# Performance work log

Hardware: AMD Instinct MI355X
Metric: run time of the kernel (lower is better)

## Reference

```python
import jax, jax.numpy as jnp
import numpy as np

ALPHA = 0.1
STEPS = 4


def setup_inputs() -> dict:
    key = jax.random.key(0)
    x = jax.random.normal(key, (4, 8192, 1024), dtype=jnp.float32)
    return {"x": x}


def reference(x) -> jnp.ndarray:
    # CtaPostAttnMixer.forward, layout='bld', prefill, steps=4, alpha=0.1
    # Fixed-boundary 1D heat-diffusion stencil along the sequence dim.
    if x.shape[1] < 3:
        return x
    y = x.astype(jnp.float32)
    for _ in range(STEPS):
        # Laplacian on interior tokens: y[l+1] - 2 y[l] + y[l-1]
        lap = y[:, 2:, :] - 2.0 * y[:, 1:-1, :] + y[:, :-2, :]
        y = jnp.concatenate(
            [y[:, :1, :], y[:, 1:-1, :] + ALPHA * lap, y[:, -1:, :]], axis=1
        )
    return y.astype(x.dtype)
```

## Files before the change

### kernel.cpp

```cpp
#include <hip/hip_runtime.h>


namespace {

constexpr int Lr   = 8192;
constexpr int Dq   = 1024 / 4;
constexpr int Bn   = 4;
constexpr int R    = 32;
constexpr int WR   = R + 8;
constexpr int CW   = 32;
constexpr int RT   = Lr / R;
constexpr int CT   = Dq / CW;
constexpr int NXCD = 8;
constexpr int NWG  = RT * CT * Bn;

constexpr float WK0 = 0.4870f;
constexpr float WK1 = 0.2144f;
constexpr float WK2 = 0.0388f;
constexpr float WK3 = 0.0032f;
constexpr float WK4 = 0.0001f;

__device__ __forceinline__ float4 f4_add(float4 a, float4 b) {
    return make_float4(a.x + b.x, a.y + b.y, a.z + b.z, a.w + b.w);
}
__device__ __forceinline__ float4 f4_mul(float s, float4 a) {
    return make_float4(s * a.x, s * a.y, s * a.z, s * a.w);
}
__device__ __forceinline__ float4 f4_fma(float s, float4 a, float4 c) {
    return make_float4(fmaf(s, a.x, c.x), fmaf(s, a.y, c.y),
                       fmaf(s, a.z, c.z), fmaf(s, a.w, c.w));
}

__global__ __launch_bounds__(256, 7)
void mixer4_kernel(const float4* __restrict__ x, float4* __restrict__ y) {
    __shared__ float4 tile[WR][CW];

    const int lin = blockIdx.x;
    const int g   = (lin & (NXCD - 1)) * (NWG / NXCD) + (lin >> 3);
    const int rt  = g & (RT - 1);
    const int bc  = g >> 8;
    const int ct  = bc & (CT - 1);
    const int b   = bc >> 3;
    const int r0  = rt * R;

    const size_t origin = (size_t)b * Lr * Dq + (size_t)ct * CW;
    const float4* __restrict__ xt = x + origin;
    float4* __restrict__       yt = y + origin;

    const int lane = threadIdx.x & 63;
    const int wid  = threadIdx.x >> 6;

#pragma unroll
    for (int ii = 0; ii < 5; ++ii) {
        const int p = wid + ii * 4;
        int grow = r0 - 4 + 2 * p + (lane >> 5);
        grow = grow < 0 ? 0 : grow;
        grow = grow > Lr - 1 ? Lr - 1 : grow;
        const float4* src = xt + (size_t)grow * Dq + (lane & 31);
        __builtin_amdgcn_global_load_lds(
            (const __attribute__((address_space(1))) void*)src,
            (__attribute__((address_space(3))) void*)&tile[2 * p][0],
            16, 0, 0);
    }
    __syncthreads();

    const int c  = threadIdx.x & 31;
    const int gr = threadIdx.x >> 5;
    float4 win[12];
#pragma unroll
    for (int i = 0; i < 12; ++i) win[i] = tile[4 * gr + i][c];

    auto interior = [&](int j) {
        float4 acc = f4_mul(WK0, win[j + 4]);
        acc = f4_fma(WK1, f4_add(win[j + 3], win[j + 5]), acc);
        acc = f4_fma(WK2, f4_add(win[j + 2], win[j + 6]), acc);
        acc = f4_fma(WK3, f4_add(win[j + 1], win[j + 7]), acc);
        acc = f4_fma(WK4, f4_add(win[j + 0], win[j + 8]), acc);
        yt[(size_t)(r0 + 4 * gr + j) * Dq + c] = acc;
    };

    const bool low  = (rt == 0)      && (gr == 0);
    const bool high = (rt == RT - 1) && (gr == 7);

    if (low) {
        yt[0 * (size_t)Dq + c] = win[4];
        {
            float4 o = f4_mul(0.2986f, win[4]);
            o = f4_fma(0.4482f, win[5], o);
            o = f4_fma(0.2112f, win[6], o);
            o = f4_fma(0.0387f, win[7], o);
            o = f4_fma(0.0032f, win[8], o);
            o = f4_fma(0.0001f, win[9], o);
            yt[1 * (size_t)Dq + c] = o;
        }
        {
            float4 o = f4_mul(0.0454f, win[4]);
            o = f4_fma(0.2112f, win[5], o);
            o = f4_fma(0.4869f, win[6], o);
            o = f4_fma(0.2144f, win[7], o);
            o = f4_fma(0.0388f, win[8], o);
            o = f4_fma(0.0032f, win[9], o);
            o = f4_fma(0.0001f, win[10], o);
            yt[2 * (size_t)Dq + c] = o;
        }
        {
            float4 o = f4_mul(0.0034f, win[4]);
            o = f4_fma(0.0387f, win[5], o);
            o = f4_fma(0.2144f, win[6], o);
            o = f4_fma(0.4870f, win[7], o);
            o = f4_fma(0.2144f, win[8], o);
            o = f4_fma(0.0388f, win[9], o);
            o = f4_fma(0.0032f, win[10], o);
            o = f4_fma(0.0001f, win[11], o);
            yt[3 * (size_t)Dq + c] = o;
        }
    } else if (high) {
        yt[(size_t)(Lr - 1) * Dq + c] = win[7];
        {
            float4 o = f4_mul(0.2986f, win[7]);
            o = f4_fma(0.4482f, win[6], o);
            o = f4_fma(0.2112f, win[5], o);
            o = f4_fma(0.0387f, win[4], o);
            o = f4_fma(0.0032f, win[3], o);
            o = f4_fma(0.0001f, win[2], o);
            yt[(size_t)(Lr - 2) * Dq + c] = o;
        }
        {
            float4 o = f4_mul(0.0454f, win[7]);
            o = f4_fma(0.2112f, win[6], o);
            o = f4_fma(0.4869f, win[5], o);
            o = f4_fma(0.2144f, win[4], o);
            o = f4_fma(0.0388f, win[3], o);
            o = f4_fma(0.0032f, win[2], o);
            o = f4_fma(0.0001f, win[1], o);
            yt[(size_t)(Lr - 3) * Dq + c] = o;
        }
        {
            float4 o = f4_mul(0.0034f, win[7]);
            o = f4_fma(0.0387f, win[6], o);
            o = f4_fma(0.2144f, win[5], o);
            o = f4_fma(0.4870f, win[4], o);
            o = f4_fma(0.2144f, win[3], o);
            o = f4_fma(0.0388f, win[2], o);
            o = f4_fma(0.0032f, win[1], o);
            o = f4_fma(0.0001f, win[0], o);
            yt[(size_t)(Lr - 4) * Dq + c] = o;
        }
    } else {
#pragma unroll
        for (int j = 0; j < 4; ++j) interior(j);
    }
}

}

extern "C" void kernel_launch(void* const* d_in, const int* in_sizes, int n_in,
                              void* d_out, int out_size, void* d_ws, size_t ws_size,
                              hipStream_t stream) {
    const float4* x = (const float4*)d_in[0];
    float4*       y = (float4*)d_out;

    dim3 grid(NWG);
    dim3 block(256);
    hipLaunchKernelGGL(mixer4_kernel, grid, block, 0, stream, x, y);
}
```

Before: 232.5 us.

## Make each workgroup march over eight row tiles with double-buffered async LDS loads

Each workgroup now handles eight consecutive row tiles of a column strip instead of one, which cuts the grid by a factor of eight. Loads for the next tile are issued into a second LDS buffer while the current tile is computed, using explicit vmcnt waits and barriers. The aim is to overlap global load latency with compute and stores and to reduce per-workgroup launch overhead. In exchange it lowers occupancy (launch bounds 7 to 4, doubled LDS) and relies on hand-counted vmcnt values, which must also account for the outstanding global stores.

```diff
diff --git a/kernel.cpp b/kernel.cpp
--- a/kernel.cpp
+++ b/kernel.cpp
@@ -11,8 +11,9 @@
 constexpr int CW   = 32;
 constexpr int RT   = Lr / R;
 constexpr int CT   = Dq / CW;
+constexpr int MT   = 8;
 constexpr int NXCD = 8;
-constexpr int NWG  = RT * CT * Bn;
+constexpr int NWG  = RT * CT * Bn / MT;
 
 constexpr float WK0 = 0.4870f;
 constexpr float WK1 = 0.2144f;
@@ -20,6 +21,9 @@
 constexpr float WK3 = 0.0032f;
 constexpr float WK4 = 0.0001f;
 
+#define WAITCNT_VM(n) asm volatile("s_waitcnt vmcnt(" #n ")" ::: "memory")
+#define MEMFENCE()    asm volatile("" ::: "memory")
+
 __device__ __forceinline__ float4 f4_add(float4 a, float4 b) {
     return make_float4(a.x + b.x, a.y + b.y, a.z + b.z, a.w + b.w);
 }
@@ -31,17 +35,17 @@
                        fmaf(s, a.z, c.z), fmaf(s, a.w, c.w));
 }
 
-__global__ __launch_bounds__(256, 7)
+__global__ __launch_bounds__(256, 4)
 void mixer4_kernel(const float4* __restrict__ x, float4* __restrict__ y) {
-    __shared__ float4 tile[WR][CW];
-
-    const int lin = blockIdx.x;
-    const int g   = (lin & (NXCD - 1)) * (NWG / NXCD) + (lin >> 3);
-    const int rt  = g & (RT - 1);
-    const int bc  = g >> 8;
-    const int ct  = bc & (CT - 1);
-    const int b   = bc >> 3;
-    const int r0  = rt * R;
+    __shared__ float4 buf[2][WR][CW];
+
+    const int lin   = blockIdx.x;
+    const int g     = (lin & (NXCD - 1)) * (NWG / NXCD) + (lin >> 3);
+    const int strip = g >> 5;
+    const int mrch  = g & 31;
+    const int ct    = strip & (CT - 1);
+    const int b     = strip >> 3;
+    const int rt0   = mrch * MT;
 
     const size_t origin = (size_t)b * Lr * Dq + (size_t)ct * CW;
     const float4* __restrict__ xt = x + origin;
@@ -50,105 +54,136 @@
     const int lane = threadIdx.x & 63;
     const int wid  = threadIdx.x >> 6;
 
+    auto stage = [&](int rt, int sel) {
+        const int r0s = rt * R;
 #pragma unroll
-    for (int ii = 0; ii < 5; ++ii) {
-        const int p = wid + ii * 4;
-        int grow = r0 - 4 + 2 * p + (lane >> 5);
-        grow = grow < 0 ? 0 : grow;
-        grow = grow > Lr - 1 ? Lr - 1 : grow;
-        const float4* src = xt + (size_t)grow * Dq + (lane & 31);
-        __builtin_amdgcn_global_load_lds(
-            (const __attribute__((address_space(1))) void*)src,
-            (__attribute__((address_space(3))) void*)&tile[2 * p][0],
-            16, 0, 0);
-    }
-    __syncthreads();
+        for (int ii = 0; ii < 5; ++ii) {
+            const int p = wid + ii * 4;
+            int grow = r0s - 4 + 2 * p + (lane >> 5);
+            grow = grow < 0 ? 0 : grow;
+            grow = grow > Lr - 1 ? Lr - 1 : grow;
+            const float4* src = xt + (size_t)grow * Dq + (lane & 31);
+            __builtin_amdgcn_global_load_lds(
+                (const __attribute__((address_space(1))) void*)src,
+                (__attribute__((address_space(3))) void*)&buf[sel][2 * p][0],
+                16, 0, 0);
+        }
+    };
 
     const int c  = threadIdx.x & 31;
     const int gr = threadIdx.x >> 5;
-    float4 win[12];
+    auto compute = [&](int rt, int sel) {
+        const int r0 = rt * R;
+        float4 win[12];
 #pragma unroll
-    for (int i = 0; i < 12; ++i) win[i] = tile[4 * gr + i][c];
-
-    auto interior = [&](int j) {
-        float4 acc = f4_mul(WK0, win[j + 4]);
-        acc = f4_fma(WK1, f4_add(win[j + 3], win[j + 5]), acc);
-        acc = f4_fma(WK2, f4_add(win[j + 2], win[j + 6]), acc);
-        acc = f4_fma(WK3, f4_add(win[j + 1], win[j + 7]), acc);
-        acc = f4_fma(WK4, f4_add(win[j + 0], win[j + 8]), acc);
-        yt[(size_t)(r0 + 4 * gr + j) * Dq + c] = acc;
+        for (int i = 0; i < 12; ++i) win[i] = buf[sel][4 * gr + i][c];
+
+        auto interior = [&](int j) {
+            float4 acc = f4_mul(WK0, win[j + 4]);
+            acc = f4_fma(WK1, f4_add(win[j + 3], win[j + 5]), acc);
+            acc = f4_fma(WK2, f4_add(win[j + 2], win[j + 6]), acc);
+            acc = f4_fma(WK3, f4_add(win[j + 1], win[j + 7]), acc);
+            acc = f4_fma(WK4, f4_add(win[j + 0], win[j + 8]), acc);
+            yt[(size_t)(r0 + 4 * gr + j) * Dq + c] = acc;
+        };
+
+        const bool low  = (rt == 0)      && (gr == 0);
+        const bool high = (rt == RT - 1) && (gr == 7);
+
+        if (low) {
+            yt[0 * (size_t)Dq + c] = win[4];
+            {
+                float4 o = f4_mul(0.2986f, win[4]);
+                o = f4_fma(0.4482f, win[5], o);
+                o = f4_fma(0.2112f, win[6], o);
+                o = f4_fma(0.0387f, win[7], o);
+                o = f4_fma(0.0032f, win[8], o);
+                o = f4_fma(0.0001f, win[9], o);
+                yt[1 * (size_t)Dq + c] = o;
+            }
+            {
+                float4 o = f4_mul(0.0454f, win[4]);
+                o = f4_fma(0.2112f, win[5], o);
+                o = f4_fma(0.4869f, win[6], o);
+                o = f4_fma(0.2144f, win[7], o);
+                o = f4_fma(0.0388f, win[8], o);
+                o = f4_fma(0.0032f, win[9], o);
+                o = f4_fma(0.0001f, win[10], o);
+                yt[2 * (size_t)Dq + c] = o;
+            }
+            {
+                float4 o = f4_mul(0.0034f, win[4]);
+                o = f4_fma(0.0387f, win[5], o);
+                o = f4_fma(0.2144f, win[6], o);
+                o = f4_fma(0.4870f, win[7], o);
+                o = f4_fma(0.2144f, win[8], o);
+                o = f4_fma(0.0388f, win[9], o);
+                o = f4_fma(0.0032f, win[10], o);
+                o = f4_fma(0.0001f, win[11], o);
+                yt[3 * (size_t)Dq + c] = o;
+            }
+        } else if (high) {
+            yt[(size_t)(Lr - 1) * Dq + c] = win[7];
+            {
+                float4 o = f4_mul(0.2986f, win[7]);
+                o = f4_fma(0.4482f, win[6], o);
+                o = f4_fma(0.2112f, win[5], o);
+                o = f4_fma(0.0387f, win[4], o);
+                o = f4_fma(0.0032f, win[3], o);
+                o = f4_fma(0.0001f, win[2], o);
+                yt[(size_t)(Lr - 2) * Dq + c] = o;
+            }
+            {
+                float4 o = f4_mul(0.0454f, win[7]);
+                o = f4_fma(0.2112f, win[6], o);
+                o = f4_fma(0.4869f, win[5], o);
+                o = f4_fma(0.2144f, win[4], o);
+                o = f4_fma(0.0388f, win[3], o);
+                o = f4_fma(0.0032f, win[2], o);
+                o = f4_fma(0.0001f, win[1], o);
+                yt[(size_t)(Lr - 3) * Dq + c] = o;
+            }
+            {
+                float4 o = f4_mul(0.0034f, win[7]);
+                o = f4_fma(0.0387f, win[6], o);
+                o = f4_fma(0.2144f, win[5], o);
+                o = f4_fma(0.4870f, win[4], o);
+                o = f4_fma(0.2144f, win[3], o);
+                o = f4_fma(0.0388f, win[2], o);
+                o = f4_fma(0.0032f, win[1], o);
+                o = f4_fma(0.0001f, win[0], o);
+                yt[(size_t)(Lr - 4) * Dq + c] = o;
+            }
+        } else {
+#pragma unroll
+            for (int j = 0; j < 4; ++j) interior(j);
+        }
     };
 
-    const bool low  = (rt == 0)      && (gr == 0);
-    const bool high = (rt == RT - 1) && (gr == 7);
-
-    if (low) {
-        yt[0 * (size_t)Dq + c] = win[4];
-        {
-            float4 o = f4_mul(0.2986f, win[4]);
-            o = f4_fma(0.4482f, win[5], o);
-            o = f4_fma(0.2112f, win[6], o);
-            o = f4_fma(0.0387f, win[7], o);
-            o = f4_fma(0.0032f, win[8], o);
-            o = f4_fma(0.0001f, win[9], o);
-            yt[1 * (size_t)Dq + c] = o;
+    stage(rt0 + 0, 0);
+    stage(rt0 + 1, 1);
+    WAITCNT_VM(5);
+    __builtin_amdgcn_s_barrier();
+    MEMFENCE();
+    compute(rt0 + 0, 0);
+    MEMFENCE();
+    __builtin_amdgcn_s_barrier();
+    MEMFENCE();
+
+    for (int t = 1; t < MT; ++t) {
+        const int cur = t & 1;
+        if (t + 1 < MT) {
+            stage(rt0 + t + 1, cur ^ 1);
+            WAITCNT_VM(9);
+        } else {
+            WAITCNT_VM(4);
         }
-        {
-            float4 o = f4_mul(0.0454f, win[4]);
-            o = f4_fma(0.2112f, win[5], o);
-            o = f4_fma(0.4869f, win[6], o);
-            o = f4_fma(0.2144f, win[7], o);
-            o = f4_fma(0.0388f, win[8], o);
-            o = f4_fma(0.0032f, win[9], o);
-            o = f4_fma(0.0001f, win[10], o);
-            yt[2 * (size_t)Dq + c] = o;
-        }
-        {
-            float4 o = f4_mul(0.0034f, win[4]);
-            o = f4_fma(0.0387f, win[5], o);
-            o = f4_fma(0.2144f, win[6], o);
-            o = f4_fma(0.4870f, win[7], o);
-            o = f4_fma(0.2144f, win[8], o);
-            o = f4_fma(0.0388f, win[9], o);
-            o = f4_fma(0.0032f, win[10], o);
-            o = f4_fma(0.0001f, win[11], o);
-            yt[3 * (size_t)Dq + c] = o;
-        }
-    } else if (high) {
-        yt[(size_t)(Lr - 1) * Dq + c] = win[7];
-        {
-            float4 o = f4_mul(0.2986f, win[7]);
-            o = f4_fma(0.4482f, win[6], o);
-            o = f4_fma(0.2112f, win[5], o);
-            o = f4_fma(0.0387f, win[4], o);
-            o = f4_fma(0.0032f, win[3], o);
-            o = f4_fma(0.0001f, win[2], o);
-            yt[(size_t)(Lr - 2) * Dq + c] = o;
-        }
-        {
-            float4 o = f4_mul(0.0454f, win[7]);
-            o = f4_fma(0.2112f, win[6], o);
-            o = f4_fma(0.4869f, win[5], o);
-            o = f4_fma(0.2144f, win[4], o);
-            o = f4_fma(0.0388f, win[3], o);
-            o = f4_fma(0.0032f, win[2], o);
-            o = f4_fma(0.0001f, win[1], o);
-            yt[(size_t)(Lr - 3) * Dq + c] = o;
-        }
-        {
-            float4 o = f4_mul(0.0034f, win[7]);
-            o = f4_fma(0.0387f, win[6], o);
-            o = f4_fma(0.2144f, win[5], o);
-            o = f4_fma(0.4870f, win[4], o);
-            o = f4_fma(0.2144f, win[3], o);
-            o = f4_fma(0.0388f, win[2], o);
-            o = f4_fma(0.0032f, win[1], o);
-            o = f4_fma(0.0001f, win[0], o);
-            yt[(size_t)(Lr - 4) * Dq + c] = o;
-        }
-    } else {
-#pragma unroll
-        for (int j = 0; j < 4; ++j) interior(j);
+        __builtin_amdgcn_s_barrier();
+        MEMFENCE();
+        compute(rt0 + t, cur);
+        MEMFENCE();
+        __builtin_amdgcn_s_barrier();
+        MEMFENCE();
     }
 }
 
```

Result: no change. 236.1 us (+1.5%).
